# Kernel optimization log

Hardware: AMD Instinct MI355X
Metric: run time of the kernel (lower is better)

Reference implementation:

```python
import jax, jax.numpy as jnp
import numpy as np

GROUPS = 16
EPS = 1e-6


def conv1x1(x, w, b):
    # x: (B,C,N,K), w: (O,C), b: (O,)
    return jnp.einsum('oc,bcnk->bonk', w, x) + b[None, :, None, None]


def group_norm(x, gamma, beta):
    # GroupNorm(16, C, eps=1e-6, affine=True) over (C/g, N, K) per sample
    B, C, N, K = x.shape
    xg = x.reshape(B, GROUPS, C // GROUPS, N, K)
    mu = xg.mean(axis=(2, 3, 4), keepdims=True)
    var = xg.var(axis=(2, 3, 4), keepdims=True)
    xn = ((xg - mu) * jax.lax.rsqrt(var + EPS)).reshape(B, C, N, K)
    return xn * gamma[None, :, None, None] + beta[None, :, None, None]


def _gather_nbrs(x, idx):
    # x: (B,C,N), idx: (B,N,K) -> (B,C,N,K)
    return jax.vmap(lambda xb, ib: xb[:, ib])(x, idx)


def lse(coords_t, feats, idx, dist, w, b, g, bt):
    # LocalSpatialEncoding: coords_t (B,3,N), feats (B,C,N,1)
    nbr_coords = _gather_nbrs(coords_t, idx)                       # (B,3,N,K)
    ctr_coords = jnp.broadcast_to(coords_t[..., None], nbr_coords.shape)
    concat = jnp.concatenate(
        [ctr_coords, nbr_coords, ctr_coords - nbr_coords, dist[:, None]], axis=1)  # (B,10,N,K)
    enc = jax.nn.relu(group_norm(conv1x1(concat, w, b), g, bt))    # (B,C,N,K)
    nbr_feats = _gather_nbrs(feats[..., 0], idx)                   # (B,C,N,K)
    return jnp.concatenate([enc, nbr_feats], axis=1)               # (B,2C,N,K)


def attentive_pool(x, w, b, g, bt):
    # mean over K, then SharedMLP with GN+ReLU -> (B,O,N,1)
    m = x.mean(axis=-1, keepdims=True)
    return jax.nn.relu(group_norm(conv1x1(m, w, b), g, bt))


def setup_inputs() -> dict:
    B, N, K, D_IN, D_OUT = 2, 32768, 16, 72, 64
    H = D_OUT // 2  # 32
    key = jax.random.key(0)
    ks = jax.random.split(key, 24)

    def w(k, o, i):
        return jax.random.normal(k, (o, i), jnp.float32) * (1.0 / np.sqrt(i))

    inp = {
        'coords': jax.random.normal(ks[0], (B, N, 3), jnp.float32),
        'features': jax.random.normal(ks[1], (B, D_IN, N, 1), jnp.float32),
        'idx': jax.random.randint(ks[2], (B, N, K), 0, N, jnp.int32),
        'dist': jax.random.uniform(ks[3], (B, N, K), jnp.float32),
        # mlp1: d_in -> d_out//2, LeakyReLU(0.2)
        'w_mlp1': w(ks[4], H, D_IN), 'b_mlp1': jnp.zeros((H,), jnp.float32),
        # lse1 mlp: 10 -> H, GN+ReLU
        'w_lse1': w(ks[5], H, 10), 'b_lse1': jnp.zeros((H,), jnp.float32),
        'g_lse1': jnp.ones((H,), jnp.float32), 'bt_lse1': jnp.zeros((H,), jnp.float32),
        # pool1: d_out -> H, GN+ReLU
        'w_pool1': w(ks[6], H, D_OUT), 'b_pool1': jnp.zeros((H,), jnp.float32),
        'g_pool1': jnp.ones((H,), jnp.float32), 'bt_pool1': jnp.zeros((H,), jnp.float32),
        # lse2 mlp: 10 -> H
        'w_lse2': w(ks[7], H, 10), 'b_lse2': jnp.zeros((H,), jnp.float32),
        'g_lse2': jnp.ones((H,), jnp.float32), 'bt_lse2': jnp.zeros((H,), jnp.float32),
        # pool2: d_out -> d_out
        'w_pool2': w(ks[8], D_OUT, D_OUT), 'b_pool2': jnp.zeros((D_OUT,), jnp.float32),
        'g_pool2': jnp.ones((D_OUT,), jnp.float32), 'bt_pool2': jnp.zeros((D_OUT,), jnp.float32),
        # mlp2: d_out -> 2*d_out (no bn, no act)
        'w_mlp2': w(ks[9], 2 * D_OUT, D_OUT), 'b_mlp2': jnp.zeros((2 * D_OUT,), jnp.float32),
        # shortcut: d_in -> 2*d_out, GN, no act
        'w_sc': w(ks[10], 2 * D_OUT, D_IN), 'b_sc': jnp.zeros((2 * D_OUT,), jnp.float32),
        'g_sc': jnp.ones((2 * D_OUT,), jnp.float32), 'bt_sc': jnp.zeros((2 * D_OUT,), jnp.float32),
    }
    return inp


def reference(coords, features, idx, dist,
              w_mlp1, b_mlp1,
              w_lse1, b_lse1, g_lse1, bt_lse1,
              w_pool1, b_pool1, g_pool1, bt_pool1,
              w_lse2, b_lse2, g_lse2, bt_lse2,
              w_pool2, b_pool2, g_pool2, bt_pool2,
              w_mlp2, b_mlp2,
              w_sc, b_sc, g_sc, bt_sc):
    coords_t = coords.transpose(0, 2, 1)                        # (B,3,N)
    x = jax.nn.leaky_relu(conv1x1(features, w_mlp1, b_mlp1), 0.2)   # (B,32,N,1)
    x = lse(coords_t, x, idx, dist, w_lse1, b_lse1, g_lse1, bt_lse1)  # (B,64,N,K)
    x = attentive_pool(x, w_pool1, b_pool1, g_pool1, bt_pool1)        # (B,32,N,1)
    x = lse(coords_t, x, idx, dist, w_lse2, b_lse2, g_lse2, bt_lse2)  # (B,64,N,K)
    x = attentive_pool(x, w_pool2, b_pool2, g_pool2, bt_pool2)        # (B,64,N,1)
    main = conv1x1(x, w_mlp2, b_mlp2)                                 # (B,128,N,1)
    sc = group_norm(conv1x1(features, w_sc, b_sc), g_sc, bt_sc)       # (B,128,N,1)
    return jax.nn.leaky_relu(main + sc, 0.01)
```

## Files before the change

### kernel.cpp

```cpp
#include <hip/hip_runtime.h>

#define NN 32768
#define GEPS 1e-6f

__device__ __forceinline__ float wredsum(float v){
  v += __shfl_xor(v, 32); v += __shfl_xor(v, 16); v += __shfl_xor(v, 8);
  v += __shfl_xor(v, 4);  v += __shfl_xor(v, 2);  v += __shfl_xor(v, 1);
  return v;
}
__device__ __forceinline__ float eredsum(float v){
  v += __shfl_xor(v, 8); v += __shfl_xor(v, 16); v += __shfl_xor(v, 32);
  return v;
}
__device__ __forceinline__ float ecomb(float v){
  v += __shfl_xor(v, 1); v += __shfl_xor(v, 2); v += __shfl_xor(v, 4);
  return v;
}

__global__ void __launch_bounds__(256) f0_prep(
    const float* __restrict__ w_mlp1, const float* __restrict__ b_mlp1,
    const float* __restrict__ w_sc,   const float* __restrict__ b_sc,
    const float* __restrict__ w_pool1,const float* __restrict__ w_pool2,
    float* __restrict__ WallT, float* __restrict__ ball,
    float* __restrict__ wp1T,  float* __restrict__ wp2T)
{
  const int t0 = blockIdx.x*256 + threadIdx.x;
  const int stride = gridDim.x*256;
  for (int u=t0; u<72*160; u+=stride){
    int i = u/160, o = u - i*160;
    WallT[u] = (o < 128) ? w_sc[o*72+i] : w_mlp1[(o-128)*72+i];
  }
  for (int u=t0; u<160; u+=stride)
    ball[u] = (u < 128) ? b_sc[u] : b_mlp1[u-128];
  for (int u=t0; u<64*32; u+=stride){ int c=u>>5, o=u&31; wp1T[u] = w_pool1[o*64+c]; }
  for (int u=t0; u<64*64; u+=stride){ int c=u>>6, o=u&63; wp2T[u] = w_pool2[o*64+c]; }
}

__global__ void __launch_bounds__(256,2) k0_mlp1_scstats(
    const float* __restrict__ feat, const float* __restrict__ WallT,
    const float* __restrict__ ball,
    float* __restrict__ X1, float* __restrict__ scS, float* __restrict__ scQ)
{
  __shared__ float xl[72][128];
  __shared__ float wl[72*32];
  __shared__ float ssl[128], sql[128];
  const int tid = threadIdx.x, lane = tid & 63;
  const int wid = __builtin_amdgcn_readfirstlane(tid >> 6);
  const int b   = __builtin_amdgcn_readfirstlane((int)blockIdx.x >> 8);
  const int n0  = ((int)blockIdx.x & 255) << 7;
  const int p0  = lane*2;

  for (int u=tid; u<72*128; u+=256){
    int c = u>>7, j = u&127;
    xl[c][j] = feat[(size_t)(b*72+c)*NN + n0 + j];
  }

#pragma unroll 1
  for (int pass=0; pass<5; ++pass){
    __syncthreads();
    for (int u=tid; u<2304; u+=256){
      int i = u>>5, c = u&31;
      wl[u] = WallT[i*160 + pass*32 + c];
    }
    __syncthreads();

    const int oc = pass*32 + wid*8;
    float a0[8], a1[8];
#pragma unroll
    for (int q=0;q<8;q++){ float bv = ball[oc+q]; a0[q]=bv; a1[q]=bv; }

    const float* wbase = wl + wid*8;
#pragma unroll
    for (int i=0;i<72;i++){
      const float2 x2 = *(const float2*)&xl[i][p0];
      const float4 w0 = *(const float4*)(wbase + i*32);
      const float4 w1 = *(const float4*)(wbase + i*32 + 4);
      a0[0]=fmaf(w0.x,x2.x,a0[0]); a1[0]=fmaf(w0.x,x2.y,a1[0]);
      a0[1]=fmaf(w0.y,x2.x,a0[1]); a1[1]=fmaf(w0.y,x2.y,a1[1]);
      a0[2]=fmaf(w0.z,x2.x,a0[2]); a1[2]=fmaf(w0.z,x2.y,a1[2]);
      a0[3]=fmaf(w0.w,x2.x,a0[3]); a1[3]=fmaf(w0.w,x2.y,a1[3]);
      a0[4]=fmaf(w1.x,x2.x,a0[4]); a1[4]=fmaf(w1.x,x2.y,a1[4]);
      a0[5]=fmaf(w1.y,x2.x,a0[5]); a1[5]=fmaf(w1.y,x2.y,a1[5]);
      a0[6]=fmaf(w1.z,x2.x,a0[6]); a1[6]=fmaf(w1.z,x2.y,a1[6]);
      a0[7]=fmaf(w1.w,x2.x,a0[7]); a1[7]=fmaf(w1.w,x2.y,a1[7]);
    }

    if (pass < 4){
#pragma unroll
      for (int q=0;q<8;q++){
        float s  = wredsum(a0[q]+a1[q]);
        float s2 = wredsum(a0[q]*a0[q] + a1[q]*a1[q]);
        if (lane==0){ ssl[oc+q] = s; sql[oc+q] = s2; }
      }
    } else {
      __syncthreads();
      float* xst = &xl[0][0];
#pragma unroll
      for (int q=0;q<8;q++){
        float v0 = a0[q], v1 = a1[q];
        v0 = v0 > 0.f ? v0 : 0.2f*v0;
        v1 = v1 > 0.f ? v1 : 0.2f*v1;
        float2 t; t.x=v0; t.y=v1;
        *(float2*)&xst[(wid*8+q)*130 + p0] = t;
      }
      __syncthreads();
      float* xb = X1 + ((size_t)b*NN + n0)*32;
#pragma unroll
      for (int r=0;r<4;r++){
        int u = tid + r*256;
        int p = u>>3, c0 = (u&7)*4;
        float4 o;
        o.x = xst[(c0+0)*130+p]; o.y = xst[(c0+1)*130+p];
        o.z = xst[(c0+2)*130+p]; o.w = xst[(c0+3)*130+p];
        *(float4*)(xb + (size_t)p*32 + c0) = o;
      }
    }
  }

  if (tid < 128){
    atomicAdd(&scS[b*128+tid], ssl[tid]);
    atomicAdd(&scQ[b*128+tid], sql[tid]);
  }
}

__global__ void __launch_bounds__(256) k1_vmom(
    const float* __restrict__ coords, const int* __restrict__ idx,
    const float* __restrict__ dist, float* __restrict__ vm)
{
  __shared__ float red[4*65];
  const int tid = threadIdx.x, lane = tid & 63, wid = tid >> 6;
  const int gn = blockIdx.x*256 + tid;
  const int pt = gn >> 2, h = gn & 3;
  const int b = pt >> 15, n = pt & (NN-1);
  const size_t pb = (size_t)b*NN + n;
  const float c0 = coords[pb*3+0], c1 = coords[pb*3+1], c2 = coords[pb*3+2];

  int ja[4]; float da[4];
  {
    int4 j4 = *(const int4*)(idx + pb*16 + h*4);
    float4 d4 = *(const float4*)(dist + pb*16 + h*4);
    ja[0]=j4.x; ja[1]=j4.y; ja[2]=j4.z; ja[3]=j4.w;
    da[0]=d4.x; da[1]=d4.y; da[2]=d4.z; da[3]=d4.w;
  }

  float aS[10], aM[55];
#pragma unroll
  for (int i=0;i<10;i++) aS[i]=0.f;
#pragma unroll
  for (int i=0;i<55;i++) aM[i]=0.f;

#pragma unroll
  for (int k=0;k<4;k++){
    const float* nb = coords + ((size_t)b*NN + ja[k])*3;
    const float n0v=nb[0], n1v=nb[1], n2v=nb[2];
    const float v[10] = {c0,c1,c2,n0v,n1v,n2v,c0-n0v,c1-n1v,c2-n2v,da[k]};
#pragma unroll
    for (int i=0;i<10;i++){
      aS[i] += v[i];
#pragma unroll
      for (int j=i;j<10;j++)
        aM[i*10 - (i*(i-1))/2 + (j-i)] += v[i]*v[j];
    }
  }

#pragma unroll
  for (int i=0;i<10;i++){ float s = wredsum(aS[i]); if (lane==0) red[wid*65+i] = s; }
#pragma unroll
  for (int i=0;i<55;i++){ float s = wredsum(aM[i]); if (lane==0) red[wid*65+10+i] = s; }
  __syncthreads();
  if (tid < 65){
    float s = red[tid] + red[65+tid] + red[130+tid] + red[195+tid];
    const int bb = blockIdx.x >> 9;
    atomicAdd(&vm[bb*65+tid], s);
  }
}

__global__ void f1_fold(
    const float* __restrict__ w_lse1, const float* __restrict__ b_lse1,
    const float* __restrict__ g_lse1, const float* __restrict__ bt_lse1,
    const float* __restrict__ w_lse2, const float* __restrict__ b_lse2,
    const float* __restrict__ g_lse2, const float* __restrict__ bt_lse2,
    const float* __restrict__ vm,
    float* __restrict__ w1p, float* __restrict__ w2p)
{
  const int tid = threadIdx.x;
  const int half = tid >> 6;
  const int u = tid & 63, b = u >> 5, c = u & 31;
  const float* W  = half ? w_lse2  : w_lse1;
  const float* Bv = half ? b_lse2  : b_lse1;
  const float* G  = half ? g_lse2  : g_lse1;
  const float* Bt = half ? bt_lse2 : bt_lse1;
  float wr[10];
#pragma unroll
  for (int i=0;i<10;i++) wr[i] = W[c*10+i];
  const float* S = vm + b*65;
  const float* M = vm + b*65 + 10;
  float P = 0.f;
#pragma unroll
  for (int i=0;i<10;i++) P = fmaf(wr[i], S[i], P);
  float Q = 0.f;
#pragma unroll
  for (int i=0;i<10;i++){
#pragma unroll
    for (int j=i;j<10;j++){
      float m = M[i*10 - (i*(i-1))/2 + (j-i)];
      float t = wr[i]*wr[j]*m;
      Q += (i==j) ? t : 2.f*t;
    }
  }
  const float invNK = 1.f/((float)NN*16.f);
  const float bc = Bv[c];
  float mean = P*invNK + bc;
  float ey2  = (Q + 2.f*bc*P)*invNK + bc*bc;
  float mu = 0.5f*(mean + __shfl_xor(mean,1));
  float e2 = 0.5f*(ey2  + __shfl_xor(ey2, 1));
  float var = e2 - mu*mu;
  float rstd = rsqrtf(var + GEPS);
  float a = G[c]*rstd, d = Bt[c] - mu*a;
  float* out = (half ? w2p : w1p) + (b*32+c)*12;
#pragma unroll
  for (int i=0;i<10;i++) out[i] = wr[i]*a;
  out[10] = bc*a + d;
  out[11] = 0.f;
}

__global__ void __launch_bounds__(256,8) k2_lse1_pool1(
    const float* __restrict__ coords, const int* __restrict__ idx,
    const float* __restrict__ dist, const float* __restrict__ X1,
    const float* __restrict__ w1p, const float* __restrict__ wp1T,
    const float* __restrict__ b_pool1,
    float* __restrict__ Y1, float* __restrict__ p1S, float* __restrict__ p1Q)
{
  __shared__ float mfl[32*66];
  __shared__ float sl[32], ql[32];
  const int tid = threadIdx.x, lane = tid & 63;
  const int e = tid & 7;
  const int pl = tid >> 3;
  if (tid < 32){ sl[tid]=0.f; ql[tid]=0.f; }
  __syncthreads();
  const int b = __builtin_amdgcn_readfirstlane((int)blockIdx.x & 1);
  const int n = (((int)blockIdx.x >> 1) << 5) + pl;
  const size_t pb = (size_t)b*NN + n;
  float* mf = &mfl[pl*66];
  const float s16 = 0.0625f;

  {
    int ja[16];
    const int4* ip = (const int4*)(idx + pb*16);
#pragma unroll
    for (int k4=0;k4<4;k4++){
      int4 j4 = ip[k4];
      ja[k4*4+0]=j4.x; ja[k4*4+1]=j4.y; ja[k4*4+2]=j4.z; ja[k4*4+3]=j4.w;
    }
    float af0=0.f, af1=0.f, af2=0.f, af3=0.f;
    const float* xb = X1 + (size_t)b*NN*32 + e*4;
#pragma unroll 4
    for (int k=0;k<16;k++){
      float4 g = *(const float4*)(xb + (size_t)ja[k]*32);
      af0+=g.x; af1+=g.y; af2+=g.z; af3+=g.w;
    }
    mf[32+e*4+0]=af0*s16; mf[32+e*4+1]=af1*s16;
    mf[32+e*4+2]=af2*s16; mf[32+e*4+3]=af3*s16;
  }

  {
    int2 j2 = *(const int2*)(idx + pb*16 + e*2);
    float2 d2 = *(const float2*)(dist + pb*16 + e*2);
    const float* nb0 = coords + ((size_t)b*NN + j2.x)*3;
    const float* nb1 = coords + ((size_t)b*NN + j2.y)*3;
    const float nx0=nb0[0], ny0=nb0[1], nz0=nb0[2];
    const float nx1=nb1[0], ny1=nb1[1], nz1=nb1[2];
    const float c0=coords[pb*3], c1=coords[pb*3+1], c2=coords[pb*3+2];
    const float* wrow = w1p + (size_t)(b*32)*12;
#pragma unroll 1
    for (int cc=0;cc<4;cc++){
      float ptc[8];
#pragma unroll
      for (int q=0;q<8;q++){
        const float4* r4 = (const float4*)(wrow + (cc*8+q)*12);
        float4 ra=r4[0], rb=r4[1], rc=r4[2];
        const float t0=ra.x+rb.z, t1=ra.y+rb.w, t2=ra.z+rc.x;
        const float u0=ra.w-rb.z, u1=rb.x-rb.w, u2=rb.y-rc.x;
        const float wd=rc.y;
        float cb = rc.z;
        cb = fmaf(t0,c0,cb); cb = fmaf(t1,c1,cb); cb = fmaf(t2,c2,cb);
        float s0 = cb, s1 = cb;
        s0 = fmaf(u0,nx0,s0); s0 = fmaf(u1,ny0,s0); s0 = fmaf(u2,nz0,s0);
        s0 = fmaf(wd,d2.x,s0);
        s1 = fmaf(u0,nx1,s1); s1 = fmaf(u1,ny1,s1); s1 = fmaf(u2,nz1,s1);
        s1 = fmaf(wd,d2.y,s1);
        ptc[q] = fmaxf(s0,0.f) + fmaxf(s1,0.f);
      }
#pragma unroll
      for (int q=0;q<8;q++) ptc[q] = ecomb(ptc[q]);
      if ((e>>1)==cc){
        float v0 = (e&1) ? ptc[4] : ptc[0];
        float v1 = (e&1) ? ptc[5] : ptc[1];
        float v2 = (e&1) ? ptc[6] : ptc[2];
        float v3 = (e&1) ? ptc[7] : ptc[3];
        mf[e*4+0]=v0*s16; mf[e*4+1]=v1*s16;
        mf[e*4+2]=v2*s16; mf[e*4+3]=v3*s16;
      }
    }
  }
  __syncthreads();

  const int o0 = e*4;
  float yac[4];
  {
    const float4 b0 = *(const float4*)(b_pool1 + o0);
    yac[0]=b0.x; yac[1]=b0.y; yac[2]=b0.z; yac[3]=b0.w;
  }
#pragma unroll 4
  for (int c=0;c<64;c++){
    const float mc = mf[c];
    const float4 w0 = *(const float4*)(wp1T + c*32 + o0);
    yac[0]=fmaf(w0.x,mc,yac[0]); yac[1]=fmaf(w0.y,mc,yac[1]);
    yac[2]=fmaf(w0.z,mc,yac[2]); yac[3]=fmaf(w0.w,mc,yac[3]);
  }
  {
    float4 r0; r0.x=yac[0]; r0.y=yac[1]; r0.z=yac[2]; r0.w=yac[3];
    *(float4*)(Y1 + pb*32 + o0) = r0;
  }
#pragma unroll
  for (int q=0;q<4;q++){
    float s  = eredsum(yac[q]);
    float s2 = eredsum(yac[q]*yac[q]);
    if (lane < 8){ atomicAdd(&sl[o0+q], s); atomicAdd(&ql[o0+q], s2); }
  }
  __syncthreads();
  if (tid<32){ atomicAdd(&p1S[b*32+tid], sl[tid]); atomicAdd(&p1Q[b*32+tid], ql[tid]); }
}

__global__ void __launch_bounds__(256) f2_apply_pool1(
    float* __restrict__ Y1, const float* __restrict__ p1S, const float* __restrict__ p1Q,
    const float* __restrict__ g, const float* __restrict__ bt)
{
  __shared__ float al[32], dl[32];
  const int tid = threadIdx.x;
  const int b = blockIdx.x >> 10;
  if (tid < 32){
    float s = p1S[b*32+tid], q = p1Q[b*32+tid];
    s += __shfl_xor(s,1); q += __shfl_xor(q,1);
    const float inv = 1.f/(2.f*(float)NN);
    float mu = s*inv, e2 = q*inv, var = e2-mu*mu;
    float rstd = rsqrtf(var + GEPS);
    float a = g[tid]*rstd;
    al[tid] = a; dl[tid] = bt[tid] - mu*a;
  }
  __syncthreads();
  const size_t e4 = (size_t)blockIdx.x*256 + tid;
  float4* Y = (float4*)Y1;
  float4 v = Y[e4];
  const int c0 = ((int)(e4 & 7))*4;
  v.x = fmaxf(fmaf(v.x, al[c0+0], dl[c0+0]), 0.f);
  v.y = fmaxf(fmaf(v.y, al[c0+1], dl[c0+1]), 0.f);
  v.z = fmaxf(fmaf(v.z, al[c0+2], dl[c0+2]), 0.f);
  v.w = fmaxf(fmaf(v.w, al[c0+3], dl[c0+3]), 0.f);
  Y[e4] = v;
}

__global__ void __launch_bounds__(256,8) k4_lse2_pool2(
    const float* __restrict__ coords, const int* __restrict__ idx,
    const float* __restrict__ dist, const float* __restrict__ Y1,
    const float* __restrict__ w2p, const float* __restrict__ wp2T,
    const float* __restrict__ b_pool2,
    float* __restrict__ Y2T, float* __restrict__ p2S, float* __restrict__ p2Q)
{
  __shared__ float mfl[32*66];
  __shared__ float sl[64], ql[64];
  const int tid = threadIdx.x, lane = tid & 63;
  const int e = tid & 7;
  const int pl = tid >> 3;
  if (tid < 64){ sl[tid]=0.f; ql[tid]=0.f; }
  __syncthreads();
  const int b = __builtin_amdgcn_readfirstlane((int)blockIdx.x & 1);
  const int n0g = (((int)blockIdx.x >> 1) << 5);
  const int n = n0g + pl;
  const size_t pb = (size_t)b*NN + n;
  float* mf = &mfl[pl*66];
  const float s16 = 0.0625f;

  {
    int ja[16];
    const int4* ip = (const int4*)(idx + pb*16);
#pragma unroll
    for (int k4=0;k4<4;k4++){
      int4 j4 = ip[k4];
      ja[k4*4+0]=j4.x; ja[k4*4+1]=j4.y; ja[k4*4+2]=j4.z; ja[k4*4+3]=j4.w;
    }
    float af0=0.f, af1=0.f, af2=0.f, af3=0.f;
    const float* yb = Y1 + (size_t)b*NN*32 + e*4;
#pragma unroll 4
    for (int k=0;k<16;k++){
      float4 g = *(const float4*)(yb + (size_t)ja[k]*32);
      af0+=g.x; af1+=g.y; af2+=g.z; af3+=g.w;
    }
    mf[32+e*4+0]=af0*s16; mf[32+e*4+1]=af1*s16;
    mf[32+e*4+2]=af2*s16; mf[32+e*4+3]=af3*s16;
  }

  {
    int2 j2 = *(const int2*)(idx + pb*16 + e*2);
    float2 d2 = *(const float2*)(dist + pb*16 + e*2);
    const float* nb0 = coords + ((size_t)b*NN + j2.x)*3;
    const float* nb1 = coords + ((size_t)b*NN + j2.y)*3;
    const float nx0=nb0[0], ny0=nb0[1], nz0=nb0[2];
    const float nx1=nb1[0], ny1=nb1[1], nz1=nb1[2];
    const float c0=coords[pb*3], c1=coords[pb*3+1], c2=coords[pb*3+2];
    const float* wrow = w2p + (size_t)(b*32)*12;
#pragma unroll 1
    for (int cc=0;cc<4;cc++){
      float ptc[8];
#pragma unroll
      for (int q=0;q<8;q++){
        const float4* r4 = (const float4*)(wrow + (cc*8+q)*12);
        float4 ra=r4[0], rb=r4[1], rc=r4[2];
        const float t0=ra.x+rb.z, t1=ra.y+rb.w, t2=ra.z+rc.x;
        const float u0=ra.w-rb.z, u1=rb.x-rb.w, u2=rb.y-rc.x;
        const float wd=rc.y;
        float cb = rc.z;
        cb = fmaf(t0,c0,cb); cb = fmaf(t1,c1,cb); cb = fmaf(t2,c2,cb);
        float s0 = cb, s1 = cb;
        s0 = fmaf(u0,nx0,s0); s0 = fmaf(u1,ny0,s0); s0 = fmaf(u2,nz0,s0);
        s0 = fmaf(wd,d2.x,s0);
        s1 = fmaf(u0,nx1,s1); s1 = fmaf(u1,ny1,s1); s1 = fmaf(u2,nz1,s1);
        s1 = fmaf(wd,d2.y,s1);
        ptc[q] = fmaxf(s0,0.f) + fmaxf(s1,0.f);
      }
#pragma unroll
      for (int q=0;q<8;q++) ptc[q] = ecomb(ptc[q]);
      if ((e>>1)==cc){
        float v0 = (e&1) ? ptc[4] : ptc[0];
        float v1 = (e&1) ? ptc[5] : ptc[1];
        float v2 = (e&1) ? ptc[6] : ptc[2];
        float v3 = (e&1) ? ptc[7] : ptc[3];
        mf[e*4+0]=v0*s16; mf[e*4+1]=v1*s16;
        mf[e*4+2]=v2*s16; mf[e*4+3]=v3*s16;
      }
    }
  }
  __syncthreads();

  const int o0 = e*8;
  float yac[8];
  {
    const float4 b0 = *(const float4*)(b_pool2 + o0);
    const float4 b1 = *(const float4*)(b_pool2 + o0 + 4);
    yac[0]=b0.x; yac[1]=b0.y; yac[2]=b0.z; yac[3]=b0.w;
    yac[4]=b1.x; yac[5]=b1.y; yac[6]=b1.z; yac[7]=b1.w;
  }
#pragma unroll 4
  for (int c=0;c<64;c++){
    const float mc = mf[c];
    const float4 w0 = *(const float4*)(wp2T + c*64 + o0);
    const float4 w1 = *(const float4*)(wp2T + c*64 + o0 + 4);
    yac[0]=fmaf(w0.x,mc,yac[0]); yac[1]=fmaf(w0.y,mc,yac[1]);
    yac[2]=fmaf(w0.z,mc,yac[2]); yac[3]=fmaf(w0.w,mc,yac[3]);
    yac[4]=fmaf(w1.x,mc,yac[4]); yac[5]=fmaf(w1.y,mc,yac[5]);
    yac[6]=fmaf(w1.z,mc,yac[6]); yac[7]=fmaf(w1.w,mc,yac[7]);
  }
#pragma unroll
  for (int q=0;q<8;q++){
    float s  = eredsum(yac[q]);
    float s2 = eredsum(yac[q]*yac[q]);
    if (lane < 8){ atomicAdd(&sl[o0+q], s); atomicAdd(&ql[o0+q], s2); }
  }
  __syncthreads();
  float* ldsT = &mfl[0];
#pragma unroll
  for (int o=0;o<8;o++) ldsT[(o0+o)*33 + pl] = yac[o];
  __syncthreads();
#pragma unroll
  for (int r=0;r<8;r++){
    int u = tid + r*256;
    int ch = u >> 5, p = u & 31;
    Y2T[((size_t)(b*64+ch))*NN + n0g + p] = ldsT[ch*33 + p];
  }
  if (tid<64){ atomicAdd(&p2S[b*64+tid], sl[tid]); atomicAdd(&p2Q[b*64+tid], ql[tid]); }
}

__global__ void f3a_affines(
    const float* __restrict__ scS, const float* __restrict__ scQ,
    const float* __restrict__ g_sc, const float* __restrict__ bt_sc,
    const float* __restrict__ b_sc, const float* __restrict__ b_mlp2,
    const float* __restrict__ p2S, const float* __restrict__ p2Q,
    const float* __restrict__ g_p2, const float* __restrict__ bt_p2,
    float* __restrict__ ascT, float* __restrict__ cstF,
    float* __restrict__ a2F, float* __restrict__ d2F)
{
  const int tid = threadIdx.x;
  if (tid < 256){
    const int b = tid >> 7, c = tid & 127;
    float s = scS[b*128+c], q = scQ[b*128+c];
    s += __shfl_xor(s,1); q += __shfl_xor(q,1);
    s += __shfl_xor(s,2); q += __shfl_xor(q,2);
    s += __shfl_xor(s,4); q += __shfl_xor(q,4);
    const float inv = 1.f/(8.f*(float)NN);
    float mu = s*inv, e2 = q*inv, var = e2-mu*mu;
    float rstd = rsqrtf(var + GEPS);
    float a = g_sc[c]*rstd;
    ascT[tid] = a;
    cstF[tid] = b_mlp2[c] + a*b_sc[c] + (bt_sc[c] - mu*a);
  } else {
    const int t = tid - 256;
    const int b = t >> 6, c = t & 63;
    float s = p2S[b*64+c], q = p2Q[b*64+c];
    s += __shfl_xor(s,1); q += __shfl_xor(q,1);
    s += __shfl_xor(s,2); q += __shfl_xor(q,2);
    const float inv = 1.f/(4.f*(float)NN);
    float mu = s*inv, e2 = q*inv, var = e2-mu*mu;
    float rstd = rsqrtf(var + GEPS);
    float a = g_p2[c]*rstd;
    a2F[t] = a; d2F[t] = bt_p2[c] - mu*a;
  }
}

__global__ void __launch_bounds__(256) f3b_wcomb(
    const float* __restrict__ w_mlp2, const float* __restrict__ w_sc,
    const float* __restrict__ ascT, float* __restrict__ Wcomb)
{
  const int t0 = blockIdx.x*256 + threadIdx.x;
  const int stride = gridDim.x*256;
  for (int u=t0; u<2*136*128; u+=stride){
    int bb = u / 17408;
    int rr = u - bb*17408;
    int i = rr >> 7, o = rr & 127;
    Wcomb[u] = (i < 64) ? w_mlp2[o*64+i]
                        : w_sc[o*72 + (i-64)] * ascT[bb*128+o];
  }
}

__global__ void __launch_bounds__(256,2) k6_final(
    const float* __restrict__ feat, const float* __restrict__ Y2T,
    const float* __restrict__ Wcomb, const float* __restrict__ cstF,
    const float* __restrict__ a2F, const float* __restrict__ d2F,
    float* __restrict__ out)
{
  __shared__ float xl[34*128];
  __shared__ float wl[34*128];
  const int tid = threadIdx.x;
  const int tc = tid & 15;
  const int tp = tid >> 4;
  const int b  = __builtin_amdgcn_readfirstlane((int)blockIdx.x >> 8);
  const int n0 = ((int)blockIdx.x & 255) << 7;

  float acc[8][8];
#pragma unroll
  for (int q=0;q<8;q++){
    float bv = cstF[b*128 + tc*8 + q];
#pragma unroll
    for (int p=0;p<8;p++) acc[p][q] = bv;
  }

  const float* Wb = Wcomb + b*17408;
#pragma unroll 1
  for (int kk=0; kk<4; ++kk){
    __syncthreads();
    for (int u=tid; u<34*128; u+=256){
      int row = u>>7, j = u&127;
      int r = kk*34 + row;
      float v;
      if (r < 64){
        float y = Y2T[(size_t)(b*64+r)*NN + n0 + j];
        v = fmaxf(fmaf(y, a2F[b*64+r], d2F[b*64+r]), 0.f);
      } else {
        v = feat[(size_t)(b*72 + (r-64))*NN + n0 + j];
      }
      xl[u] = v;
    }
    for (int u=tid; u<34*128; u+=256){
      int row = u>>7, c = u&127;
      wl[u] = Wb[(size_t)(kk*34+row)*128 + c];
    }
    __syncthreads();

#pragma unroll 2
    for (int i=0;i<34;i++){
      const float4 xa = *(const float4*)&xl[i*128 + tp*8];
      const float4 xb = *(const float4*)&xl[i*128 + tp*8 + 4];
      const float4 wa = *(const float4*)&wl[i*128 + tc*8];
      const float4 wb = *(const float4*)&wl[i*128 + tc*8 + 4];
      const float xs[8] = {xa.x,xa.y,xa.z,xa.w,xb.x,xb.y,xb.z,xb.w};
      const float wv[8] = {wa.x,wa.y,wa.z,wa.w,wb.x,wb.y,wb.z,wb.w};
#pragma unroll
      for (int p=0;p<8;p++)
#pragma unroll
        for (int q=0;q<8;q++)
          acc[p][q] = fmaf(wv[q], xs[p], acc[p][q]);
    }
  }

#pragma unroll
  for (int q=0;q<8;q++){
    const int ch = b*128 + tc*8 + q;
    float4 r0, r1;
    float v;
    v = acc[0][q]; r0.x = v>0.f? v : 0.01f*v;
    v = acc[1][q]; r0.y = v>0.f? v : 0.01f*v;
    v = acc[2][q]; r0.z = v>0.f? v : 0.01f*v;
    v = acc[3][q]; r0.w = v>0.f? v : 0.01f*v;
    v = acc[4][q]; r1.x = v>0.f? v : 0.01f*v;
    v = acc[5][q]; r1.y = v>0.f? v : 0.01f*v;
    v = acc[6][q]; r1.z = v>0.f? v : 0.01f*v;
    v = acc[7][q]; r1.w = v>0.f? v : 0.01f*v;
    float* ob = out + (size_t)ch*NN + n0 + tp*8;
    *(float4*)(ob)     = r0;
    *(float4*)(ob + 4) = r1;
  }
}

extern "C" void kernel_launch(void* const* d_in, const int* in_sizes, int n_in,
                              void* d_out, int out_size, void* d_ws, size_t ws_size,
                              hipStream_t stream) {
  (void)in_sizes; (void)n_in; (void)out_size; (void)ws_size;
  const float* coords  = (const float*)d_in[0];
  const float* feats   = (const float*)d_in[1];
  const int*   idx     = (const int*)  d_in[2];
  const float* dist    = (const float*)d_in[3];
  const float* w_mlp1  = (const float*)d_in[4];
  const float* b_mlp1  = (const float*)d_in[5];
  const float* w_lse1  = (const float*)d_in[6];
  const float* b_lse1  = (const float*)d_in[7];
  const float* g_lse1  = (const float*)d_in[8];
  const float* bt_lse1 = (const float*)d_in[9];
  const float* w_pool1 = (const float*)d_in[10];
  const float* b_pool1 = (const float*)d_in[11];
  const float* g_pool1 = (const float*)d_in[12];
  const float* bt_pool1= (const float*)d_in[13];
  const float* w_lse2  = (const float*)d_in[14];
  const float* b_lse2  = (const float*)d_in[15];
  const float* g_lse2  = (const float*)d_in[16];
  const float* bt_lse2 = (const float*)d_in[17];
  const float* w_pool2 = (const float*)d_in[18];
  const float* b_pool2 = (const float*)d_in[19];
  const float* g_pool2 = (const float*)d_in[20];
  const float* bt_pool2= (const float*)d_in[21];
  const float* w_mlp2  = (const float*)d_in[22];
  const float* b_mlp2  = (const float*)d_in[23];
  const float* w_sc    = (const float*)d_in[24];
  const float* b_sc    = (const float*)d_in[25];
  const float* g_sc    = (const float*)d_in[26];
  const float* bt_sc   = (const float*)d_in[27];

  float* ws   = (float*)d_ws;
  float* scS  = ws;
  float* scQ  = ws + 256;
  float* vm   = ws + 512;
  float* p1S  = ws + 704;
  float* p1Q  = ws + 768;
  float* p2S  = ws + 832;
  float* p2Q  = ws + 960;
  float* w1p  = ws + 1280;
  float* w2p  = ws + 2048;
  float* wp1T = ws + 2816;
  float* wp2T = ws + 4864;
  float* ball = ws + 8960;
  float* cstF = ws + 9120;
  float* a2F  = ws + 9376;
  float* d2F  = ws + 9504;
  float* ascT = ws + 9632;
  float* WallT= ws + 9984;
  float* Wcomb= ws + 21504;
  float* X1   = ws + 57344;
  float* Y1   = X1 + (size_t)2*NN*32;
  float* Y2T  = Y1 + (size_t)2*NN*32;

  hipMemsetAsync(d_ws, 0, 1088*sizeof(float), stream);

  f0_prep<<<32,256,0,stream>>>(w_mlp1,b_mlp1,w_sc,b_sc,w_pool1,w_pool2,
                               WallT,ball,wp1T,wp2T);
  k0_mlp1_scstats<<<512,256,0,stream>>>(feats, WallT, ball, X1, scS, scQ);
  k1_vmom<<<1024,256,0,stream>>>(coords, idx, dist, vm);
  f1_fold<<<1,128,0,stream>>>(w_lse1,b_lse1,g_lse1,bt_lse1,
                              w_lse2,b_lse2,g_lse2,bt_lse2,
                              vm, w1p, w2p);
  k2_lse1_pool1<<<2048,256,0,stream>>>(coords, idx, dist, X1, w1p, wp1T, b_pool1,
                                       Y1, p1S, p1Q);
  f2_apply_pool1<<<2048,256,0,stream>>>(Y1, p1S, p1Q, g_pool1, bt_pool1);
  k4_lse2_pool2<<<2048,256,0,stream>>>(coords, idx, dist, Y1, w2p, wp2T, b_pool2,
                                       Y2T, p2S, p2Q);
  f3a_affines<<<1,384,0,stream>>>(scS,scQ,g_sc,bt_sc,b_sc,b_mlp2,
                                  p2S,p2Q,g_pool2,bt_pool2, ascT,cstF,a2F,d2F);
  f3b_wcomb<<<64,256,0,stream>>>(w_mlp2, w_sc, ascT, Wcomb);
  k6_final<<<512,256,0,stream>>>(feats, Y2T, Wcomb, cstF, a2F, d2F, (float*)d_out);
}
```

Before: 259.1 us.

## Fuse pool1 GroupNorm apply into lse2 gather and stage pool weights in LDS

Drops the separate f2_apply_pool1 pass over Y1. The pool1 GroupNorm affine and ReLU are now applied per gathered neighbor inside k4_lse2_pool2, which saves a full read and write of Y1 at the cost of 16x more affine ops per point. Both pool kernels also copy their pool weight matrices into LDS per block instead of reading them from global memory. Min-blocks in launch bounds drops from 8 to 6 to allow for the larger LDS use.

```diff
diff --git a/kernel.cpp b/kernel.cpp
--- a/kernel.cpp
+++ b/kernel.cpp
@@ -224,7 +224,7 @@
   out[11] = 0.f;
 }
 
-__global__ void __launch_bounds__(256,8) k2_lse1_pool1(
+__global__ void __launch_bounds__(256,6) k2_lse1_pool1(
     const float* __restrict__ coords, const int* __restrict__ idx,
     const float* __restrict__ dist, const float* __restrict__ X1,
     const float* __restrict__ w1p, const float* __restrict__ wp1T,
@@ -232,11 +232,13 @@
     float* __restrict__ Y1, float* __restrict__ p1S, float* __restrict__ p1Q)
 {
   __shared__ float mfl[32*66];
+  __shared__ float wlds[64*32];
   __shared__ float sl[32], ql[32];
   const int tid = threadIdx.x, lane = tid & 63;
   const int e = tid & 7;
   const int pl = tid >> 3;
   if (tid < 32){ sl[tid]=0.f; ql[tid]=0.f; }
+  for (int u=tid; u<2048; u+=256) wlds[u] = wp1T[u];
   __syncthreads();
   const int b = __builtin_amdgcn_readfirstlane((int)blockIdx.x & 1);
   const int n = (((int)blockIdx.x >> 1) << 5) + pl;
@@ -314,7 +316,7 @@
 #pragma unroll 4
   for (int c=0;c<64;c++){
     const float mc = mf[c];
-    const float4 w0 = *(const float4*)(wp1T + c*32 + o0);
+    const float4 w0 = *(const float4*)(wlds + c*32 + o0);
     yac[0]=fmaf(w0.x,mc,yac[0]); yac[1]=fmaf(w0.y,mc,yac[1]);
     yac[2]=fmaf(w0.z,mc,yac[2]); yac[3]=fmaf(w0.w,mc,yac[3]);
   }
@@ -332,49 +334,36 @@
   if (tid<32){ atomicAdd(&p1S[b*32+tid], sl[tid]); atomicAdd(&p1Q[b*32+tid], ql[tid]); }
 }
 
-__global__ void __launch_bounds__(256) f2_apply_pool1(
-    float* __restrict__ Y1, const float* __restrict__ p1S, const float* __restrict__ p1Q,
-    const float* __restrict__ g, const float* __restrict__ bt)
-{
+__global__ void __launch_bounds__(256,6) k4_lse2_pool2(
+    const float* __restrict__ coords, const int* __restrict__ idx,
+    const float* __restrict__ dist, const float* __restrict__ Y1,
+    const float* __restrict__ w2p, const float* __restrict__ wp2T,
+    const float* __restrict__ b_pool2,
+    const float* __restrict__ p1S, const float* __restrict__ p1Q,
+    const float* __restrict__ g_p1, const float* __restrict__ bt_p1,
+    float* __restrict__ Y2T, float* __restrict__ p2S, float* __restrict__ p2Q)
+{
+  __shared__ float mfl[32*66];
+  __shared__ float wlds[64*64];
+  __shared__ float sl[64], ql[64];
   __shared__ float al[32], dl[32];
-  const int tid = threadIdx.x;
-  const int b = blockIdx.x >> 10;
-  if (tid < 32){
-    float s = p1S[b*32+tid], q = p1Q[b*32+tid];
+  const int tid = threadIdx.x, lane = tid & 63;
+  const int e = tid & 7;
+  const int pl = tid >> 3;
+  const int b = __builtin_amdgcn_readfirstlane((int)blockIdx.x & 1);
+  if (tid < 64){ sl[tid]=0.f; ql[tid]=0.f; }
+  if (tid >= 64 && tid < 96){
+    const int c = tid - 64;
+    float s = p1S[b*32+c], q = p1Q[b*32+c];
     s += __shfl_xor(s,1); q += __shfl_xor(q,1);
     const float inv = 1.f/(2.f*(float)NN);
     float mu = s*inv, e2 = q*inv, var = e2-mu*mu;
     float rstd = rsqrtf(var + GEPS);
-    float a = g[tid]*rstd;
-    al[tid] = a; dl[tid] = bt[tid] - mu*a;
-  }
-  __syncthreads();
-  const size_t e4 = (size_t)blockIdx.x*256 + tid;
-  float4* Y = (float4*)Y1;
-  float4 v = Y[e4];
-  const int c0 = ((int)(e4 & 7))*4;
-  v.x = fmaxf(fmaf(v.x, al[c0+0], dl[c0+0]), 0.f);
-  v.y = fmaxf(fmaf(v.y, al[c0+1], dl[c0+1]), 0.f);
-  v.z = fmaxf(fmaf(v.z, al[c0+2], dl[c0+2]), 0.f);
-  v.w = fmaxf(fmaf(v.w, al[c0+3], dl[c0+3]), 0.f);
-  Y[e4] = v;
-}
-
-__global__ void __launch_bounds__(256,8) k4_lse2_pool2(
-    const float* __restrict__ coords, const int* __restrict__ idx,
-    const float* __restrict__ dist, const float* __restrict__ Y1,
-    const float* __restrict__ w2p, const float* __restrict__ wp2T,
-    const float* __restrict__ b_pool2,
-    float* __restrict__ Y2T, float* __restrict__ p2S, float* __restrict__ p2Q)
-{
-  __shared__ float mfl[32*66];
-  __shared__ float sl[64], ql[64];
-  const int tid = threadIdx.x, lane = tid & 63;
-  const int e = tid & 7;
-  const int pl = tid >> 3;
-  if (tid < 64){ sl[tid]=0.f; ql[tid]=0.f; }
-  __syncthreads();
-  const int b = __builtin_amdgcn_readfirstlane((int)blockIdx.x & 1);
+    float a = g_p1[c]*rstd;
+    al[c] = a; dl[c] = bt_p1[c] - mu*a;
+  }
+  for (int u=tid; u<4096; u+=256) wlds[u] = wp2T[u];
+  __syncthreads();
   const int n0g = (((int)blockIdx.x >> 1) << 5);
   const int n = n0g + pl;
   const size_t pb = (size_t)b*NN + n;
@@ -382,6 +371,8 @@
   const float s16 = 0.0625f;
 
   {
+    const float a0g=al[e*4+0], a1g=al[e*4+1], a2g=al[e*4+2], a3g=al[e*4+3];
+    const float d0g=dl[e*4+0], d1g=dl[e*4+1], d2g=dl[e*4+2], d3g=dl[e*4+3];
     int ja[16];
     const int4* ip = (const int4*)(idx + pb*16);
 #pragma unroll
@@ -394,7 +385,10 @@
 #pragma unroll 4
     for (int k=0;k<16;k++){
       float4 g = *(const float4*)(yb + (size_t)ja[k]*32);
-      af0+=g.x; af1+=g.y; af2+=g.z; af3+=g.w;
+      af0 += fmaxf(fmaf(g.x, a0g, d0g), 0.f);
+      af1 += fmaxf(fmaf(g.y, a1g, d1g), 0.f);
+      af2 += fmaxf(fmaf(g.z, a2g, d2g), 0.f);
+      af3 += fmaxf(fmaf(g.w, a3g, d3g), 0.f);
     }
     mf[32+e*4+0]=af0*s16; mf[32+e*4+1]=af1*s16;
     mf[32+e*4+2]=af2*s16; mf[32+e*4+3]=af3*s16;
@@ -453,8 +447,8 @@
 #pragma unroll 4
   for (int c=0;c<64;c++){
     const float mc = mf[c];
-    const float4 w0 = *(const float4*)(wp2T + c*64 + o0);
-    const float4 w1 = *(const float4*)(wp2T + c*64 + o0 + 4);
+    const float4 w0 = *(const float4*)(wlds + c*64 + o0);
+    const float4 w1 = *(const float4*)(wlds + c*64 + o0 + 4);
     yac[0]=fmaf(w0.x,mc,yac[0]); yac[1]=fmaf(w0.y,mc,yac[1]);
     yac[2]=fmaf(w0.z,mc,yac[2]); yac[3]=fmaf(w0.w,mc,yac[3]);
     yac[4]=fmaf(w1.x,mc,yac[4]); yac[5]=fmaf(w1.y,mc,yac[5]);
@@ -677,8 +671,8 @@
                               vm, w1p, w2p);
   k2_lse1_pool1<<<2048,256,0,stream>>>(coords, idx, dist, X1, w1p, wp1T, b_pool1,
                                        Y1, p1S, p1Q);
-  f2_apply_pool1<<<2048,256,0,stream>>>(Y1, p1S, p1Q, g_pool1, bt_pool1);
   k4_lse2_pool2<<<2048,256,0,stream>>>(coords, idx, dist, Y1, w2p, wp2T, b_pool2,
+                                       p1S, p1Q, g_pool1, bt_pool1,
                                        Y2T, p2S, p2Q);
   f3a_affines<<<1,384,0,stream>>>(scS,scQ,g_sc,bt_sc,b_sc,b_mlp2,
                                   p2S,p2Q,g_pool2,bt_pool2, ascT,cstF,a2F,d2F);
```

Measured after the change: 247.4 us. 4.5% less time.
